# Performance work log

Measured on AMD Instinct MI355X. Metric: run time of the kernel, lower is better.

The kernel has to match this reference:

```python
import jax, jax.numpy as jnp
import numpy as np

BATCH, INPUT, SEQ = 512, 128, 256
HIDDEN, OUT = 1024, 128


def setup_inputs() -> dict:
    key = jax.random.key(0)
    ks = jax.random.split(key, 7)
    s_ih = 1.0 / np.sqrt(INPUT)
    s_hh = 1.0 / np.sqrt(HIDDEN)
    return {
        "x": jax.random.normal(ks[0], (BATCH, INPUT, SEQ), dtype=jnp.float32),
        "W_ih": jax.random.normal(ks[1], (4 * HIDDEN, INPUT), dtype=jnp.float32) * s_ih,
        "W_hh": jax.random.normal(ks[2], (4 * HIDDEN, HIDDEN), dtype=jnp.float32) * s_hh,
        "b_ih": jax.random.normal(ks[3], (4 * HIDDEN,), dtype=jnp.float32) * s_hh,
        "b_hh": jax.random.normal(ks[4], (4 * HIDDEN,), dtype=jnp.float32) * s_hh,
        "W_fc": jax.random.normal(ks[5], (OUT, HIDDEN), dtype=jnp.float32) * s_hh,
        "b_fc": jax.random.normal(ks[6], (OUT,), dtype=jnp.float32) * s_hh,
    }


def reference(x, W_ih, W_hh, b_ih, b_hh, W_fc, b_fc):
    H = W_hh.shape[1]
    # (B, I, T) -> (B, T, I); original loop processes timesteps 0 .. T-2
    xt = jnp.transpose(x, (0, 2, 1))[:, :-1, :]
    # Precompute input contribution to all gates: (T-1, B, 4H)
    gx = jnp.einsum('bti,gi->tbg', xt, W_ih) + b_ih + b_hh

    B = x.shape[0]
    h0 = jnp.zeros((B, H), dtype=x.dtype)
    c0 = jnp.zeros((B, H), dtype=x.dtype)

    def step(carry, g_in):
        h, c = carry
        gates = g_in + h @ W_hh.T  # (B, 4H); PyTorch gate order i, f, g, o
        i_g, f_g, g_g, o_g = jnp.split(gates, 4, axis=-1)
        i_g = jax.nn.sigmoid(i_g)
        f_g = jax.nn.sigmoid(f_g)
        g_g = jnp.tanh(g_g)
        o_g = jax.nn.sigmoid(o_g)
        c_new = f_g * c + i_g * g_g
        h_new = o_g * jnp.tanh(c_new)
        return (h_new, c_new), None

    (h_last, _), _ = jax.lax.scan(step, (h0, c0), gx)
    # fc on last step's output, squeeze(1) -> (B, OUT)
    return h_last @ W_fc.T + b_fc
```

## Files before the change

kernel.cpp:

```cpp
#include <hip/hip_runtime.h>
#include <stdint.h>
#include <stddef.h>

typedef __attribute__((ext_vector_type(8))) _Float16 half8;
typedef __attribute__((ext_vector_type(8))) unsigned short ushort8;
typedef __attribute__((ext_vector_type(4))) float f4;
typedef __attribute__((ext_vector_type(2))) float f2;

#define AS1 __attribute__((address_space(1)))
#define AS3 __attribute__((address_space(3)))

namespace {
constexpr int kSteps = 255;
constexpr int KTOT = 1152;

constexpr size_t OFF_H0   = 0;
constexpr size_t OFF_CNT  = (size_t)1 << 20;
constexpr size_t OFF_H1   = ((size_t)1 << 20) + 4096;
constexpr size_t OFF_BSUM = OFF_H1 + ((size_t)1 << 20);
constexpr size_t OFF_WCAT = OFF_BSUM + 16384;
constexpr size_t OFF_XT   = OFF_WCAT + (size_t)4096 * KTOT * 2;
}

__device__ __forceinline__ unsigned short f2h(float f) {
  _Float16 h = (_Float16)f;
  return __builtin_bit_cast(unsigned short, h);
}
__device__ __forceinline__ float h2f(unsigned short s) {
  return (float)__builtin_bit_cast(_Float16, s);
}

__global__ void prep_wcat(const float* __restrict__ Wih, const float* __restrict__ Whh,
                          const float* __restrict__ bih, const float* __restrict__ bhh,
                          char* __restrict__ ws) {
  if (blockIdx.x < 2304) {
    unsigned gid = blockIdx.x * 256 + threadIdx.x;
    unsigned row = gid / 144, cc = gid % 144;
    const float* src = (cc < 128) ? (Whh + (size_t)row * 1024 + (size_t)cc * 8)
                                  : (Wih + (size_t)row * 128 + (size_t)(cc - 128) * 8);
    ushort8 o;
#pragma unroll
    for (int j = 0; j < 8; j++) o[j] = f2h(src[j]);
    *(ushort8*)((unsigned short*)(ws + OFF_WCAT) + (size_t)row * KTOT + cc * 8) = o;
  } else {
    int i = (blockIdx.x - 2304) * 256 + threadIdx.x;
    ((float*)(ws + OFF_BSUM))[i] = bih[i] + bhh[i];
  }
}

__global__ void prep_xt(const float* __restrict__ x, char* __restrict__ ws) {
  unsigned short* xT = (unsigned short*)(ws + OFF_XT);
  __shared__ unsigned short tile[128][72];
  const int b = blockIdx.x >> 2;
  const int t0 = (blockIdx.x & 3) * 64;
  const int wv = threadIdx.x >> 6, tl = threadIdx.x & 63;
  if (t0 + tl < 255) {
#pragma unroll
    for (int ii = 0; ii < 32; ii++) {
      int i = wv + ii * 4;
      tile[i][tl] = f2h(x[((size_t)b * 128 + i) * 256 + t0 + tl]);
    }
  }
  __syncthreads();
  const int tl2 = threadIdx.x >> 4, ic = threadIdx.x & 15;
#pragma unroll
  for (int pp = 0; pp < 4; pp++) {
    int tloc = pp * 16 + tl2;
    int t = t0 + tloc;
    if (t < 255) {
      ushort8 v;
#pragma unroll
      for (int j = 0; j < 8; j++) v[j] = tile[ic * 8 + j][tloc];
      *(ushort8*)&xT[((size_t)t * 512 + b) * 128 + ic * 8] = v;
    }
  }
}

#define WAITBAR(N) do { \
    asm volatile("s_waitcnt vmcnt(" #N ") lgkmcnt(0)\n\ts_barrier" ::: "memory"); \
    __builtin_amdgcn_sched_barrier(0); \
  } while (0)

__global__ __launch_bounds__(512) __attribute__((amdgpu_waves_per_eu(2, 2)))
void lstm_persist(char* __restrict__ ws) {
  const unsigned short* __restrict__ wcat = (const unsigned short*)(ws + OFF_WCAT);
  const float* __restrict__ bsum = (const float*)(ws + OFF_BSUM);
  const unsigned short* __restrict__ xT = (const unsigned short*)(ws + OFF_XT);
  unsigned short* h0 = (unsigned short*)(ws + OFF_H0);
  unsigned short* h1 = (unsigned short*)(ws + OFF_H1);

  __shared__ __align__(16) char lds[131072];

  const int tid = threadIdx.x;
  const int lane = tid & 63;
  const int w = tid >> 6;
  const int wk = w & 3;
  const int wn = w >> 2;
  const int l15 = lane & 15, l4 = lane >> 4;
  const int gA = blockIdx.x & 7;
  const int gB = gA + 8;
  const int cblk = blockIdx.x >> 3;
  const int U0 = cblk * 32;
  int* cntA = (int*)(ws + OFF_CNT) + gA * 16;
  int* cntB = (int*)(ws + OFF_CNT) + gB * 16;

  half8 bf[9][4];
  float bseed[4];
#pragma unroll
  for (int nf = 0; nf < 4; nf++) {
    int u = wn * 16 + nf * 4 + (l15 >> 2);
    int R = (l15 & 3) * 1024 + U0 + u;
    float b = bsum[R];
    bseed[nf] = (wk == 0) ? b : 0.f;
#pragma unroll
    for (int c = 0; c < 9; c++)
      bf[c][nf] = *(const half8*)&wcat[(size_t)R * KTOT + c * 128 + wk * 32 + l4 * 8];
  }

  const int srow = w * 4 + (lane >> 4);
  const int scg = (lane & 15) ^ (srow & 7);
  const int hoff1 = (scg >> 2) * 1024 + srow * 32 + (scg & 3) * 8;
  const int xoA = (gA * 32 + srow) * 128 + scg * 8;
  const int xoB = (gB * 32 + srow) * 128 + scg * 8;
  const int aBase = l15 * 256 + (((wk * 4 + l4) ^ (l15 & 7)) * 16);

  int nb8[4], hnw[4];
#pragma unroll
  for (int nf = 0; nf < 4; nf++) {
    int n = wn * 64 + nf * 16 + l15;
    nb8[nf] = n * 8;
    hnw[nf] = (n ^ (n >> 3)) & 7;
  }
  const int uu = tid & 31;
  const int qr = (tid >> 5) & 7;
  const int hi = (tid >> 8) & 1;
  int ro2[4];
#pragma unroll
  for (int g2 = 0; g2 < 4; g2++) {
    int n = 4 * uu + g2;
    ro2[g2] = (n * 8 + (qr ^ ((n ^ (n >> 3)) & 7))) * 16 + hi * 8;
  }
  const size_t hbA = ((size_t)(gA * 32 + cblk) * 32 + (qr * 4 + hi * 2)) * 32 + uu;
  const size_t hbB = ((size_t)(gB * 32 + cblk) * 32 + (qr * 4 + hi * 2)) * 32 + uu;

  f4 acc[2][4];
  float cA0 = 0.f, cA1 = 0.f, cB0 = 0.f, cB1 = 0.f;

#define STG(HS, C, RB, BUF) \
  __builtin_amdgcn_global_load_lds( \
      (const AS1 void*)((HS) + hoff1 + (C) * 4096), \
      (AS3 void*)(lds + (RB) + (BUF) * 8192 + w * 1024), 16, 0, 1)

#define CMP(C, RB, BUF) do { \
    const char* _b = lds + (RB) + (BUF) * 8192 + aBase; \
    half8 a0 = *(const half8*)(_b); \
    half8 a1 = *(const half8*)(_b + 4096); \
    acc[0][0] = __builtin_amdgcn_mfma_f32_16x16x32_f16(a0, bf[C][0], acc[0][0], 0, 0, 0); \
    acc[0][1] = __builtin_amdgcn_mfma_f32_16x16x32_f16(a0, bf[C][1], acc[0][1], 0, 0, 0); \
    acc[0][2] = __builtin_amdgcn_mfma_f32_16x16x32_f16(a0, bf[C][2], acc[0][2], 0, 0, 0); \
    acc[0][3] = __builtin_amdgcn_mfma_f32_16x16x32_f16(a0, bf[C][3], acc[0][3], 0, 0, 0); \
    acc[1][0] = __builtin_amdgcn_mfma_f32_16x16x32_f16(a1, bf[C][0], acc[1][0], 0, 0, 0); \
    acc[1][1] = __builtin_amdgcn_mfma_f32_16x16x32_f16(a1, bf[C][1], acc[1][1], 0, 0, 0); \
    acc[1][2] = __builtin_amdgcn_mfma_f32_16x16x32_f16(a1, bf[C][2], acc[1][2], 0, 0, 0); \
    acc[1][3] = __builtin_amdgcn_mfma_f32_16x16x32_f16(a1, bf[C][3], acc[1][3], 0, 0, 0); \
  } while (0)

#define CHAIN_STEP(HSRCG, HDST, HB, XSLAB, XO, CNTP, RB, C0, C1, TGT) do { \
    _Pragma("unroll") \
    for (int m = 0; m < 2; m++) \
      _Pragma("unroll") \
      for (int nf = 0; nf < 4; nf++) \
        acc[m][nf] = (f4){bseed[nf], bseed[nf], bseed[nf], bseed[nf]}; \
    __builtin_amdgcn_global_load_lds((const AS1 void*)((XSLAB) + (XO)), \
        (AS3 void*)(lds + (RB) + 7 * 8192 + w * 1024), 16, 0, 0); \
    if (tid == 0) { \
      int guard = 1 << 18; \
      while (guard--) { \
        int c; \
        asm volatile("global_load_dword %0, %1, off sc0 sc1\n\ts_waitcnt vmcnt(0)" \
                     : "=v"(c) : "v"(CNTP) : "memory"); \
        if (c >= (TGT)) break; \
        __builtin_amdgcn_s_sleep(1); \
      } \
    } \
    __syncthreads(); \
    STG(HSRCG, 0, RB, 0); STG(HSRCG, 1, RB, 1); STG(HSRCG, 2, RB, 2); STG(HSRCG, 3, RB, 3); \
    CMP(8, RB, 7); \
    STG(HSRCG, 4, RB, 4); STG(HSRCG, 5, RB, 5); \
    WAITBAR(4); CMP(0, RB, 0); CMP(1, RB, 1); \
    STG(HSRCG, 6, RB, 6); STG(HSRCG, 7, RB, 7); \
    WAITBAR(4); CMP(2, RB, 2); CMP(3, RB, 3); \
    WAITBAR(2); CMP(4, RB, 4); CMP(5, RB, 5); \
    WAITBAR(0); CMP(6, RB, 6); CMP(7, RB, 7); \
    asm volatile("s_waitcnt lgkmcnt(0)\n\ts_barrier" ::: "memory"); \
    _Pragma("unroll") \
    for (int m = 0; m < 2; m++) \
      _Pragma("unroll") \
      for (int nf = 0; nf < 4; nf++) { \
        int rf = m * 4 + l4; \
        *(f4*)(lds + (RB) + wk * 16384 + (size_t)(nb8[nf] + (rf ^ hnw[nf])) * 16) = acc[m][nf]; \
      } \
    __syncthreads(); \
    { \
      f2 gsv[4]; \
      _Pragma("unroll") \
      for (int g2 = 0; g2 < 4; g2++) { \
        f2 s0 = *(const f2*)(lds + (RB) + ro2[g2]); \
        f2 s1 = *(const f2*)(lds + (RB) + 16384 + ro2[g2]); \
        f2 s2 = *(const f2*)(lds + (RB) + 32768 + ro2[g2]); \
        f2 s3 = *(const f2*)(lds + (RB) + 49152 + ro2[g2]); \
        gsv[g2] = (s0 + s1) + (s2 + s3); \
      } \
      float ig0 = 1.f / (1.f + __expf(-gsv[0][0])); \
      float fg0 = 1.f / (1.f + __expf(-gsv[1][0])); \
      float gg0 = 2.f / (1.f + __expf(-2.f * gsv[2][0])) - 1.f; \
      float og0 = 1.f / (1.f + __expf(-gsv[3][0])); \
      float cn0 = fg0 * (C0) + ig0 * gg0; \
      (C0) = cn0; \
      float th0 = 2.f / (1.f + __expf(-2.f * cn0)) - 1.f; \
      unsigned short* hp0 = (HDST) + (HB); \
      unsigned hv0 = f2h(og0 * th0); \
      asm volatile("global_store_short %0, %1, off sc0 sc1" :: "v"(hp0), "v"(hv0) : "memory"); \
      float ig1 = 1.f / (1.f + __expf(-gsv[0][1])); \
      float fg1 = 1.f / (1.f + __expf(-gsv[1][1])); \
      float gg1 = 2.f / (1.f + __expf(-2.f * gsv[2][1])) - 1.f; \
      float og1 = 1.f / (1.f + __expf(-gsv[3][1])); \
      float cn1 = fg1 * (C1) + ig1 * gg1; \
      (C1) = cn1; \
      float th1 = 2.f / (1.f + __expf(-2.f * cn1)) - 1.f; \
      unsigned short* hp1 = (HDST) + (HB) + 32; \
      unsigned hv1 = f2h(og1 * th1); \
      asm volatile("global_store_short %0, %1, off sc0 sc1" :: "v"(hp1), "v"(hv1) : "memory"); \
    } \
    __syncthreads();  \
    if (tid == 0) \
      __hip_atomic_fetch_add(CNTP, 1, __ATOMIC_RELAXED, __HIP_MEMORY_SCOPE_AGENT); \
  } while (0)

#pragma unroll 1
  for (int t = 0; t < kSteps; t++) {
    const unsigned short* hsrc = (t & 1) ? h1 : h0;
    unsigned short* hdst = (t & 1) ? h0 : h1;
    const unsigned short* xslab = xT + (size_t)t * (512 * 128);
    const int tgt = 32 * t;

    CHAIN_STEP(hsrc + gA * 32768, hdst, hbA, xslab, xoA, cntA, 0, cA0, cA1, tgt);
    CHAIN_STEP(hsrc + gB * 32768, hdst, hbB, xslab, xoB, cntB, 65536, cB0, cB1, tgt);
  }
#undef CHAIN_STEP
#undef CMP
#undef STG
}

__global__ void fc_kernel(const char* __restrict__ ws, const float* __restrict__ Wfc,
                          const float* __restrict__ bfc, float* __restrict__ out) {
  const unsigned short* h = (const unsigned short*)(ws + OFF_H1);
  int o = threadIdx.x & 127;
  int b = blockIdx.x * 2 + (threadIdx.x >> 7);
  const float* wrow = Wfc + (size_t)o * 1024;
  float acc = bfc[o];
  int gb = b >> 5, rb = b & 31;
#pragma unroll 4
  for (int k = 0; k < 1024; k += 8) {
    ushort8 hv = *(const ushort8*)&h[(((size_t)(gb * 32 + (k >> 5)) * 32 + rb) * 32) + (k & 31)];
    f4 w0 = *(const f4*)&wrow[k];
    f4 w1 = *(const f4*)&wrow[k + 4];
#pragma unroll
    for (int j = 0; j < 4; j++) acc += h2f(hv[j]) * w0[j];
#pragma unroll
    for (int j = 0; j < 4; j++) acc += h2f(hv[4 + j]) * w1[j];
  }
  out[(size_t)b * 128 + o] = acc;
}

extern "C" void kernel_launch(void* const* d_in, const int* in_sizes, int n_in,
                              void* d_out, int out_size, void* d_ws, size_t ws_size,
                              hipStream_t stream) {
  const float* x   = (const float*)d_in[0];
  const float* Wih = (const float*)d_in[1];
  const float* Whh = (const float*)d_in[2];
  const float* bih = (const float*)d_in[3];
  const float* bhh = (const float*)d_in[4];
  const float* Wfc = (const float*)d_in[5];
  const float* bfc = (const float*)d_in[6];
  char* ws = (char*)d_ws;

  hipMemsetAsync(ws + OFF_H0, 0, ((size_t)1 << 20) + 4096, stream);
  prep_wcat<<<2320, 256, 0, stream>>>(Wih, Whh, bih, bhh, ws);
  prep_xt<<<2048, 256, 0, stream>>>(x, ws);
  lstm_persist<<<256, 512, 0, stream>>>(ws);
  fc_kernel<<<256, 256, 0, stream>>>(ws, Wfc, bfc, (float*)d_out);
}
```

Baseline: 1.913 ms.

## Software-pipeline two batch chains so h staging overlaps the other chain's epilogue

Restructures the persistent LSTM loop so that the spin-wait and the global-to-LDS staging of the hidden state for one batch group are issued before the other group's gate exchange and cell update. The hidden loads for the next step of chain A are prefetched while chain B finishes. The fine-grained per-chunk wait/barrier interleave inside each step is dropped. The x-input slab is now loaded straight into registers instead of through LDS. The aim is to hide global load latency and the inter-block sync wait behind independent work. The cost is that the fully staged ring must land before compute starts, and the ordering of LDS reuse between the two regions grows more complex.

Measured after the change: 1.824 ms. 1.05x faster.

```diff
diff --git a/kernel.cpp b/kernel.cpp
--- a/kernel.cpp
+++ b/kernel.cpp
@@ -75,11 +75,6 @@
     }
   }
 }
-
-#define WAITBAR(N) do { \
-    asm volatile("s_waitcnt vmcnt(" #N ") lgkmcnt(0)\n\ts_barrier" ::: "memory"); \
-    __builtin_amdgcn_sched_barrier(0); \
-  } while (0)
 
 __global__ __launch_bounds__(512) __attribute__((amdgpu_waves_per_eu(2, 2)))
 void lstm_persist(char* __restrict__ ws) {
@@ -120,9 +115,8 @@
   const int srow = w * 4 + (lane >> 4);
   const int scg = (lane & 15) ^ (srow & 7);
   const int hoff1 = (scg >> 2) * 1024 + srow * 32 + (scg & 3) * 8;
-  const int xoA = (gA * 32 + srow) * 128 + scg * 8;
-  const int xoB = (gB * 32 + srow) * 128 + scg * 8;
   const int aBase = l15 * 256 + (((wk * 4 + l4) ^ (l15 & 7)) * 16);
+  const int xco = (wk * 4 + l4) * 8;
 
   int nb8[4], hnw[4];
 #pragma unroll
@@ -144,6 +138,7 @@
   const size_t hbB = ((size_t)(gB * 32 + cblk) * 32 + (qr * 4 + hi * 2)) * 32 + uu;
 
   f4 acc[2][4];
+  half8 xa0, xa1, xb0, xb1;
   float cA0 = 0.f, cA1 = 0.f, cB0 = 0.f, cB1 = 0.f;
 
 #define STG(HS, C, RB, BUF) \
@@ -151,28 +146,44 @@
       (const AS1 void*)((HS) + hoff1 + (C) * 4096), \
       (AS3 void*)(lds + (RB) + (BUF) * 8192 + w * 1024), 16, 0, 1)
 
-#define CMP(C, RB, BUF) do { \
-    const char* _b = lds + (RB) + (BUF) * 8192 + aBase; \
+#define STG_RING(HS, RB) do { \
+    STG(HS, 0, RB, 0); STG(HS, 1, RB, 1); STG(HS, 2, RB, 2); STG(HS, 3, RB, 3); \
+    STG(HS, 4, RB, 4); STG(HS, 5, RB, 5); STG(HS, 6, RB, 6); STG(HS, 7, RB, 7); \
+  } while (0)
+
+#define MFMA8(A0, A1, C) do { \
+    acc[0][0] = __builtin_amdgcn_mfma_f32_16x16x32_f16(A0, bf[C][0], acc[0][0], 0, 0, 0); \
+    acc[0][1] = __builtin_amdgcn_mfma_f32_16x16x32_f16(A0, bf[C][1], acc[0][1], 0, 0, 0); \
+    acc[0][2] = __builtin_amdgcn_mfma_f32_16x16x32_f16(A0, bf[C][2], acc[0][2], 0, 0, 0); \
+    acc[0][3] = __builtin_amdgcn_mfma_f32_16x16x32_f16(A0, bf[C][3], acc[0][3], 0, 0, 0); \
+    acc[1][0] = __builtin_amdgcn_mfma_f32_16x16x32_f16(A1, bf[C][0], acc[1][0], 0, 0, 0); \
+    acc[1][1] = __builtin_amdgcn_mfma_f32_16x16x32_f16(A1, bf[C][1], acc[1][1], 0, 0, 0); \
+    acc[1][2] = __builtin_amdgcn_mfma_f32_16x16x32_f16(A1, bf[C][2], acc[1][2], 0, 0, 0); \
+    acc[1][3] = __builtin_amdgcn_mfma_f32_16x16x32_f16(A1, bf[C][3], acc[1][3], 0, 0, 0); \
+  } while (0)
+
+#define CMP(C, RB) do { \
+    const char* _b = lds + (RB) + (C) * 8192 + aBase; \
     half8 a0 = *(const half8*)(_b); \
     half8 a1 = *(const half8*)(_b + 4096); \
-    acc[0][0] = __builtin_amdgcn_mfma_f32_16x16x32_f16(a0, bf[C][0], acc[0][0], 0, 0, 0); \
-    acc[0][1] = __builtin_amdgcn_mfma_f32_16x16x32_f16(a0, bf[C][1], acc[0][1], 0, 0, 0); \
-    acc[0][2] = __builtin_amdgcn_mfma_f32_16x16x32_f16(a0, bf[C][2], acc[0][2], 0, 0, 0); \
-    acc[0][3] = __builtin_amdgcn_mfma_f32_16x16x32_f16(a0, bf[C][3], acc[0][3], 0, 0, 0); \
-    acc[1][0] = __builtin_amdgcn_mfma_f32_16x16x32_f16(a1, bf[C][0], acc[1][0], 0, 0, 0); \
-    acc[1][1] = __builtin_amdgcn_mfma_f32_16x16x32_f16(a1, bf[C][1], acc[1][1], 0, 0, 0); \
-    acc[1][2] = __builtin_amdgcn_mfma_f32_16x16x32_f16(a1, bf[C][2], acc[1][2], 0, 0, 0); \
-    acc[1][3] = __builtin_amdgcn_mfma_f32_16x16x32_f16(a1, bf[C][3], acc[1][3], 0, 0, 0); \
-  } while (0)
-
-#define CHAIN_STEP(HSRCG, HDST, HB, XSLAB, XO, CNTP, RB, C0, C1, TGT) do { \
+    MFMA8(a0, a1, C); \
+  } while (0)
+
+#define COMPUTE_ALL(RB, XA0, XA1) do { \
+    MFMA8(XA0, XA1, 8); \
+    CMP(0, RB); CMP(1, RB); CMP(2, RB); CMP(3, RB); \
+    CMP(4, RB); CMP(5, RB); CMP(6, RB); CMP(7, RB); \
+  } while (0)
+
+#define INIT_ACC do { \
     _Pragma("unroll") \
     for (int m = 0; m < 2; m++) \
       _Pragma("unroll") \
       for (int nf = 0; nf < 4; nf++) \
         acc[m][nf] = (f4){bseed[nf], bseed[nf], bseed[nf], bseed[nf]}; \
-    __builtin_amdgcn_global_load_lds((const AS1 void*)((XSLAB) + (XO)), \
-        (AS3 void*)(lds + (RB) + 7 * 8192 + w * 1024), 16, 0, 0); \
+  } while (0)
+
+#define SPIN(CNTP, TGT) do { \
     if (tid == 0) { \
       int guard = 1 << 18; \
       while (guard--) { \
@@ -183,16 +194,10 @@
         __builtin_amdgcn_s_sleep(1); \
       } \
     } \
-    __syncthreads(); \
-    STG(HSRCG, 0, RB, 0); STG(HSRCG, 1, RB, 1); STG(HSRCG, 2, RB, 2); STG(HSRCG, 3, RB, 3); \
-    CMP(8, RB, 7); \
-    STG(HSRCG, 4, RB, 4); STG(HSRCG, 5, RB, 5); \
-    WAITBAR(4); CMP(0, RB, 0); CMP(1, RB, 1); \
-    STG(HSRCG, 6, RB, 6); STG(HSRCG, 7, RB, 7); \
-    WAITBAR(4); CMP(2, RB, 2); CMP(3, RB, 3); \
-    WAITBAR(2); CMP(4, RB, 4); CMP(5, RB, 5); \
-    WAITBAR(0); CMP(6, RB, 6); CMP(7, RB, 7); \
-    asm volatile("s_waitcnt lgkmcnt(0)\n\ts_barrier" ::: "memory"); \
+    __syncthreads();  \
+  } while (0)
+
+#define EXCHFIN(RB, HDST, HB, C0, C1, CNTP) do { \
     _Pragma("unroll") \
     for (int m = 0; m < 2; m++) \
       _Pragma("unroll") \
@@ -237,18 +242,47 @@
       __hip_atomic_fetch_add(CNTP, 1, __ATOMIC_RELAXED, __HIP_MEMORY_SCOPE_AGENT); \
   } while (0)
 
+  STG_RING(h0 + gA * 32768, 0);
+  {
+    const unsigned short* xp = xT + (gA * 32 + l15) * 128 + xco;
+    xa0 = *(const half8*)xp; xa1 = *(const half8*)(xp + 2048);
+  }
+  __syncthreads();
+
 #pragma unroll 1
   for (int t = 0; t < kSteps; t++) {
     const unsigned short* hsrc = (t & 1) ? h1 : h0;
     unsigned short* hdst = (t & 1) ? h0 : h1;
-    const unsigned short* xslab = xT + (size_t)t * (512 * 128);
-    const int tgt = 32 * t;
-
-    CHAIN_STEP(hsrc + gA * 32768, hdst, hbA, xslab, xoA, cntA, 0, cA0, cA1, tgt);
-    CHAIN_STEP(hsrc + gB * 32768, hdst, hbB, xslab, xoB, cntB, 65536, cB0, cB1, tgt);
-  }
-#undef CHAIN_STEP
+
+    INIT_ACC;
+    COMPUTE_ALL(0, xa0, xa1);
+    SPIN(cntB, 32 * t);
+    STG_RING(hsrc + gB * 32768, 65536);
+    {
+      const unsigned short* xp = xT + (size_t)t * 65536 + (gB * 32 + l15) * 128 + xco;
+      xb0 = *(const half8*)xp; xb1 = *(const half8*)(xp + 2048);
+    }
+    EXCHFIN(0, hdst, hbA, cA0, cA1, cntA);
+
+    INIT_ACC;
+    COMPUTE_ALL(65536, xb0, xb1);
+    if (t + 1 < kSteps) {
+      SPIN(cntA, 32 * (t + 1));
+      STG_RING(hdst + gA * 32768, 0);
+      const unsigned short* xp = xT + (size_t)(t + 1) * 65536 + (gA * 32 + l15) * 128 + xco;
+      xa0 = *(const half8*)xp; xa1 = *(const half8*)(xp + 2048);
+    } else {
+      __syncthreads();
+    }
+    EXCHFIN(65536, hdst, hbB, cB0, cB1, cntB);
+  }
+#undef EXCHFIN
+#undef SPIN
+#undef INIT_ACC
+#undef COMPUTE_ALL
 #undef CMP
+#undef MFMA8
+#undef STG_RING
 #undef STG
 }
 
```
